# Kernel optimization log

Measured on AMD Instinct MI355X. Metric: run time of the kernel, lower is better.

The kernel has to match this reference:

```python
import jax, jax.numpy as jnp
import numpy as np

C = 256
RED = 2
C2 = C // RED


def setup_inputs() -> dict:
    key = jax.random.key(0)
    ks = jax.random.split(key, 6)
    B, H, W = 8, 64, 64
    x = jax.random.normal(ks[0], (B, C, H, W), dtype=jnp.float32)
    # 1x1 convs stored as [out_ch, in_ch] matrices
    W1 = jax.random.normal(ks[1], (C2, C), dtype=jnp.float32) * (1.0 / np.sqrt(C))
    b1 = jax.random.normal(ks[2], (C2,), dtype=jnp.float32) * 0.01
    W2 = jax.random.normal(ks[3], (C, C2), dtype=jnp.float32) * (1.0 / np.sqrt(C2))
    b2 = jax.random.normal(ks[4], (C,), dtype=jnp.float32) * 0.01
    # torch inits scale to zeros; use randn so the residual branch is active
    scale = jax.random.normal(ks[5], (1, C, 1, 1), dtype=jnp.float32)
    return {"x": x, "W1": W1, "b1": b1, "W2": W2, "b2": b2, "scale": scale}


def reference(x, W1, b1, W2, b2, scale):
    B, Cc, H, Wd = x.shape
    # conv1 (1x1): [B,C,H,W] -> [B,C2,H,W]
    y = jnp.einsum('bchw,oc->bohw', x, W1) + b1[None, :, None, None]
    # flatten spatial, move channels last: [B, N, C2]
    y = y.reshape(B, C2, H * Wd).transpose(0, 2, 1)
    # unscaled self-attention over N spatial positions
    att = jax.nn.softmax(jnp.einsum('bmc,bnc->bmn', y, y), axis=-1)  # [B,N,N]
    out = jnp.einsum('bmn,bnc->bmc', att, y)  # [B,N,C2]
    # faithful to torch: raw .view(B,-1,H,W) WITHOUT permuting back
    out = out.reshape(B, C2, H, Wd)
    # conv2 (1x1): [B,C2,H,W] -> [B,C,H,W]
    out = jnp.einsum('bchw,oc->bohw', out, W2) + b2[None, :, None, None]
    return out * scale + x
```

## Files before the change

### kernel.cpp

```cpp
#include <hip/hip_runtime.h>

#define B_  8
#define C_  256
#define C2_ 128
#define N_  4096
#define LOG2E 1.44269504088896f

typedef _Float16 f16;
typedef _Float16 f16x8 __attribute__((ext_vector_type(8)));
typedef float f32x4  __attribute__((ext_vector_type(4)));

__global__ __launch_bounds__(256)
void prep_kernel(const float* __restrict__ W1, const float* __restrict__ W2,
                 f16* __restrict__ w1h, f16* __restrict__ w2h)
{
  int i = blockIdx.x * 256 + threadIdx.x;
  w1h[i] = (f16)W1[i];
  w2h[i] = (f16)W2[i];
}

__global__ __launch_bounds__(256, 3)
void conv1_kernel(const float* __restrict__ x,
                  const f16* __restrict__ w1h,
                  const float* __restrict__ b1,
                  f16* __restrict__ Y, f16* __restrict__ Yt)
{
  __shared__ __align__(16) char smem[49152];
  float* Xr = (float*)smem;
  f16*   Ah = (f16*)(smem + 32768);
  f16*   T  = (f16*)smem;

  const int t = threadIdx.x;
  const int w = t >> 6, lane = t & 63, quad = lane >> 4, l16 = lane & 15;
  const int b = blockIdx.x, nt0 = blockIdx.y;

#pragma unroll
  for (int pass = 0; pass < 8; pass++) {
    int c  = (t >> 3) + pass * 32;
    int n4 = t & 7;
    float4 v = *(const float4*)(x + ((long)(b * C_ + c)) * N_ + nt0 * 32 + n4 * 4);
    *(float4*)(&Xr[c * 32 + (n4 ^ (c & 7)) * 4]) = v;
  }
  __syncthreads();
#pragma unroll
  for (int pass = 0; pass < 4; pass++) {
    int n  = t & 31;
    int kb = (t >> 5) + pass * 8;
    f16x8 vh;
#pragma unroll
    for (int jj = 0; jj < 8; jj++) {
      int cc = kb * 8 + jj;
      vh[jj] = (f16)Xr[cc * 32 + ((n >> 2) ^ (cc & 7)) * 4 + (n & 3)];
    }
    *(f16x8*)(&Ah[n * 256 + (kb ^ (n & 7)) * 8]) = vh;
  }
  __syncthreads();

  f16x8 bh[2][8];
#pragma unroll
  for (int nt = 0; nt < 2; nt++) {
    int c2 = w * 32 + nt * 16 + l16;
#pragma unroll
    for (int ks = 0; ks < 8; ks++)
      bh[nt][ks] = *(const f16x8*)(w1h + c2 * C_ + ks * 32 + quad * 8);
  }

  f32x4 acc[2][2];
#pragma unroll
  for (int i = 0; i < 2; i++)
#pragma unroll
    for (int j = 0; j < 2; j++) acc[i][j] = (f32x4){0.f, 0.f, 0.f, 0.f};

#pragma unroll
  for (int ks = 0; ks < 8; ks++)
#pragma unroll
    for (int mt = 0; mt < 2; mt++) {
      f16x8 ah = *(const f16x8*)(&Ah[(mt * 16 + l16) * 256 + (((ks * 4 + quad) ^ (l16 & 7))) * 8]);
#pragma unroll
      for (int nt = 0; nt < 2; nt++)
        acc[mt][nt] = __builtin_amdgcn_mfma_f32_16x16x32_f16(ah, bh[nt][ks], acc[mt][nt], 0, 0, 0);
    }
  __syncthreads();

#pragma unroll
  for (int nt = 0; nt < 2; nt++) {
    int c2 = w * 32 + nt * 16 + l16;
    float bv = b1[c2];
#pragma unroll
    for (int mt = 0; mt < 2; mt++)
#pragma unroll
      for (int rg = 0; rg < 4; rg++) {
        int n = mt * 16 + quad * 4 + rg;
        T[c2 * 40 + n] = (f16)(acc[mt][nt][rg] + bv);
      }
  }
  __syncthreads();
#pragma unroll
  for (int pass = 0; pass < 2; pass++) {
    int r  = (t >> 2) + pass * 64;
    int c8 = (t & 3) * 8;
    f16x8 v = *(const f16x8*)(&T[r * 40 + c8]);
    *(f16x8*)(Yt + ((long)(b * C2_ + r)) * N_ + nt0 * 32 + c8) = v;
  }
#pragma unroll
  for (int pass = 0; pass < 2; pass++) {
    int row = t & 31;
    int cg  = (t >> 5) + pass * 8;
    f16x8 v;
#pragma unroll
    for (int jj = 0; jj < 8; jj++) v[jj] = T[(cg * 8 + jj) * 40 + row];
    *(f16x8*)(Y + ((long)(b * N_ + nt0 * 32 + row)) * C2_ + cg * 8) = v;
  }
}

__global__ __launch_bounds__(256, 2)
void attn_kernel(const f16* __restrict__ Y, const f16* __restrict__ Yt,
                 f16* __restrict__ Op, float* __restrict__ ls)
{
  __shared__ f16 Ks[64 * 128];
  __shared__ f16 Vs[128 * 64];
  __shared__ f16 Ps[128 * 64];

  const int t = threadIdx.x;
  const int w = t >> 6, lane = t & 63, quad = lane >> 4, l16 = lane & 15;
  const int b = blockIdx.x, qt = blockIdx.y, s = blockIdx.z;
  const f16* Yb  = Y  + (long)b * N_ * C2_;
  const f16* Ytb = Yt + (long)b * C2_ * N_;
  const int kbase0 = s * 2048;

  f16x8 qf[2][4];
#pragma unroll
  for (int mt = 0; mt < 2; mt++)
#pragma unroll
    for (int ks = 0; ks < 4; ks++)
      qf[mt][ks] = *(const f16x8*)(Yb + (long)(qt * 128 + w * 32 + mt * 16 + l16) * C2_ + ks * 32 + quad * 8);

  {
    float* nsqf = (float*)Ps;
    int r = t >> 1, half = t & 1;
    float ss = 0.f;
#pragma unroll
    for (int j = 0; j < 8; j++) {
      f16x8 v = *(const f16x8*)(Yb + (long)(qt * 128 + r) * C2_ + half * 64 + j * 8);
#pragma unroll
      for (int e = 0; e < 8; e++) { float f = (float)v[e]; ss = fmaf(f, f, ss); }
    }
    ss += __shfl_xor(ss, 1);
    if (!(t & 1)) nsqf[r] = ss;
  }

#pragma unroll
  for (int pass = 0; pass < 4; pass++) {
    int r = (t >> 4) + pass * 16;
    f16x8 kv = *(const f16x8*)(Yb + (long)(kbase0 + r) * C2_ + (t & 15) * 8);
    *(f16x8*)(&Ks[r * 128 + (((t & 15)) ^ (r & 15)) * 8]) = kv;
  }
#pragma unroll
  for (int pass = 0; pass < 4; pass++) {
    int d = (t >> 3) + pass * 32;
    f16x8 vv = *(const f16x8*)(Ytb + (long)d * N_ + kbase0 + (t & 7) * 8);
    *(f16x8*)(&Vs[d * 64 + (((t & 7)) ^ (d & 7)) * 8]) = vv;
  }
  __syncthreads();

  float myns[2][4];
  {
    const float* nsqf = (const float*)Ps;
#pragma unroll
    for (int mt = 0; mt < 2; mt++)
#pragma unroll
      for (int rg = 0; rg < 4; rg++)
        myns[mt][rg] = nsqf[w * 32 + mt * 16 + quad * 4 + rg] * LOG2E;
  }
  __syncthreads();

  f16x8 ones;
#pragma unroll
  for (int j = 0; j < 8; j++) ones[j] = (f16)1.0f;

  f32x4 Oa[2][8];
#pragma unroll
  for (int i = 0; i < 2; i++)
#pragma unroll
    for (int j = 0; j < 8; j++) Oa[i][j] = (f32x4){0.f, 0.f, 0.f, 0.f};
  f32x4 lac[2] = {(f32x4){0.f,0.f,0.f,0.f}, (f32x4){0.f,0.f,0.f,0.f}};

#pragma unroll 1
  for (int kt = 0; kt < 32; kt++) {
    f16x8 stK[4], stV[4];
    if (kt + 1 < 32) {
      int nb = kbase0 + (kt + 1) * 64;
#pragma unroll
      for (int pass = 0; pass < 4; pass++)
        stK[pass] = *(const f16x8*)(Yb + (long)(nb + (t >> 4) + pass * 16) * C2_ + (t & 15) * 8);
#pragma unroll
      for (int pass = 0; pass < 4; pass++)
        stV[pass] = *(const f16x8*)(Ytb + (long)((t >> 3) + pass * 32) * N_ + nb + (t & 7) * 8);
    }

    f32x4 S[2][4];
#pragma unroll
    for (int i = 0; i < 2; i++)
#pragma unroll
      for (int j = 0; j < 4; j++) S[i][j] = (f32x4){0.f, 0.f, 0.f, 0.f};
#pragma unroll
    for (int ks = 0; ks < 4; ks++) {
      f16x8 bfr[4];
#pragma unroll
      for (int nt = 0; nt < 4; nt++)
        bfr[nt] = *(const f16x8*)(&Ks[(nt * 16 + l16) * 128 + (((ks * 4 + quad) ^ l16)) * 8]);
#pragma unroll
      for (int mt = 0; mt < 2; mt++)
#pragma unroll
        for (int nt = 0; nt < 4; nt++)
          S[mt][nt] = __builtin_amdgcn_mfma_f32_16x16x32_f16(qf[mt][ks], bfr[nt], S[mt][nt], 0, 0, 0);
    }

#pragma unroll
    for (int mt = 0; mt < 2; mt++)
#pragma unroll
      for (int rg = 0; rg < 4; rg++) {
        float nm = myns[mt][rg];
        int r = w * 32 + mt * 16 + quad * 4 + rg;
#pragma unroll
        for (int nt = 0; nt < 4; nt++) {
          float p = exp2f(fminf(fmaf(S[mt][nt][rg], LOG2E, -nm), 11.0f));
          int col = nt * 16 + l16;
          Ps[r * 64 + (((col >> 3) ^ (r & 7))) * 8 + (col & 7)] = (f16)p;
        }
      }

#pragma unroll
    for (int ks2 = 0; ks2 < 2; ks2++) {
      f16x8 vb[8];
#pragma unroll
      for (int dt = 0; dt < 8; dt++)
        vb[dt] = *(const f16x8*)(&Vs[(dt * 16 + l16) * 64 + (((ks2 * 4 + quad) ^ (l16 & 7))) * 8]);
      f16x8 pa[2];
#pragma unroll
      for (int mt = 0; mt < 2; mt++)
        pa[mt] = *(const f16x8*)(&Ps[(w * 32 + mt * 16 + l16) * 64 + (((ks2 * 4 + quad) ^ (l16 & 7))) * 8]);
#pragma unroll
      for (int mt = 0; mt < 2; mt++) {
#pragma unroll
        for (int dt = 0; dt < 8; dt++)
          Oa[mt][dt] = __builtin_amdgcn_mfma_f32_16x16x32_f16(pa[mt], vb[dt], Oa[mt][dt], 0, 0, 0);
        lac[mt] = __builtin_amdgcn_mfma_f32_16x16x32_f16(pa[mt], ones, lac[mt], 0, 0, 0);
      }
    }

    __syncthreads();
    if (kt + 1 < 32) {
#pragma unroll
      for (int pass = 0; pass < 4; pass++) {
        int r = (t >> 4) + pass * 16;
        *(f16x8*)(&Ks[r * 128 + (((t & 15)) ^ (r & 15)) * 8]) = stK[pass];
      }
#pragma unroll
      for (int pass = 0; pass < 4; pass++) {
        int d = (t >> 3) + pass * 32;
        *(f16x8*)(&Vs[d * 64 + (((t & 7)) ^ (d & 7)) * 8]) = stV[pass];
      }
    }
    __syncthreads();
  }

  const long rbase = ((long)s * B_ + b) * N_ + qt * 128;
#pragma unroll
  for (int mt = 0; mt < 2; mt++)
#pragma unroll
    for (int rg = 0; rg < 4; rg++) {
      int r = w * 32 + mt * 16 + quad * 4 + rg;
#pragma unroll
      for (int dt = 0; dt < 8; dt++)
        Op[(rbase + r) * C2_ + dt * 16 + l16] = (f16)Oa[mt][dt][rg];
      if (l16 == 0) ls[rbase + r] = lac[mt][rg];
    }
}

__global__ __launch_bounds__(256, 4)
void conv2_kernel(const f16* __restrict__ Op, const float* __restrict__ ls,
                  const f16* __restrict__ w2h,
                  const float* __restrict__ b2,
                  const float* __restrict__ scale,
                  const float* __restrict__ x,
                  float* __restrict__ out)
{
  __shared__ f16 Or[128 * 72];
  __shared__ f16 Bsw[64 * 128];
  __shared__ float invL[128];

  const int t = threadIdx.x;
  const int w = t >> 6, lane = t & 63, quad = lane >> 4, l16 = lane & 15;
  const int b = blockIdx.x, pt = blockIdx.y, oh = blockIdx.z;
  const long base0 = (long)b * 524288;
  const long base1 = 4194304 + base0;

  if (t < 128) {
    int q = t * 32 + (pt >> 1);
    float l = ls[(long)b * N_ + q] + ls[32768 + (long)b * N_ + q];
    invL[t] = 1.0f / fmaxf(l, 1e-20f);
  }
  __syncthreads();

#pragma unroll
  for (int pass = 0; pass < 4; pass++) {
    int j = (t >> 3) + pass * 32;
    int c8 = (t & 7) * 8;
    f16x8 a0 = *(const f16x8*)(Op + base0 + (long)j * N_ + pt * 64 + c8);
    f16x8 a1 = *(const f16x8*)(Op + base1 + (long)j * N_ + pt * 64 + c8);
    float iv = invL[j];
    f16x8 r;
#pragma unroll
    for (int jj = 0; jj < 8; jj++)
      r[jj] = (f16)(((float)a0[jj] + (float)a1[jj]) * iv);
    *(f16x8*)(&Or[j * 72 + c8]) = r;
  }
  __syncthreads();
#pragma unroll
  for (int pass = 0; pass < 4; pass++) {
    int p = t & 63;
    int q = (t >> 6) + pass * 4;
    f16x8 vv;
#pragma unroll
    for (int jj = 0; jj < 8; jj++) vv[jj] = Or[(q * 8 + jj) * 72 + p];
    *(f16x8*)(&Bsw[p * 128 + ((q ^ (p & 15))) * 8]) = vv;
  }
  __syncthreads();

  f32x4 acc[2][4];
#pragma unroll
  for (int i = 0; i < 2; i++)
#pragma unroll
    for (int j = 0; j < 4; j++) acc[i][j] = (f32x4){0.f, 0.f, 0.f, 0.f};

#pragma unroll
  for (int ks = 0; ks < 4; ks++) {
    f16x8 bfr[4];
#pragma unroll
    for (int nt = 0; nt < 4; nt++)
      bfr[nt] = *(const f16x8*)(&Bsw[(nt * 16 + l16) * 128 + (((ks * 4 + quad) ^ l16)) * 8]);
#pragma unroll
    for (int mt = 0; mt < 2; mt++) {
      int o = oh * 128 + w * 32 + mt * 16 + l16;
      f16x8 ah = *(const f16x8*)(w2h + o * C2_ + ks * 32 + quad * 8);
#pragma unroll
      for (int nt = 0; nt < 4; nt++)
        acc[mt][nt] = __builtin_amdgcn_mfma_f32_16x16x32_f16(ah, bfr[nt], acc[mt][nt], 0, 0, 0);
    }
  }
#pragma unroll
  for (int mt = 0; mt < 2; mt++)
#pragma unroll
    for (int rg = 0; rg < 4; rg++) {
      int o = oh * 128 + w * 32 + mt * 16 + quad * 4 + rg;
      float so = scale[o], bo = b2[o];
#pragma unroll
      for (int nt = 0; nt < 4; nt++) {
        int p = pt * 64 + nt * 16 + l16;
        long xo = ((long)b * C_ + o) * N_ + p;
        out[xo] = (acc[mt][nt][rg] + bo) * so + x[xo];
      }
    }
}

extern "C" void kernel_launch(void* const* d_in, const int* in_sizes, int n_in,
                              void* d_out, int out_size, void* d_ws, size_t ws_size,
                              hipStream_t stream) {
  const float* x     = (const float*)d_in[0];
  const float* W1    = (const float*)d_in[1];
  const float* b1    = (const float*)d_in[2];
  const float* W2    = (const float*)d_in[3];
  const float* b2    = (const float*)d_in[4];
  const float* scale = (const float*)d_in[5];
  float* outp = (float*)d_out;

  const size_t NE = (size_t)B_ * N_ * C2_;
  f16* Y   = (f16*)d_ws;
  f16* Yt  = Y + NE;
  f16* Op  = Yt + NE;
  float* ls = (float*)(Op + 2 * NE);
  f16* w1h = (f16*)(ls + 65536);
  f16* w2h = w1h + 32768;

  prep_kernel <<<dim3(128),      dim3(256), 0, stream>>>(W1, W2, w1h, w2h);
  conv1_kernel<<<dim3(8, 128),   dim3(256), 0, stream>>>(x, w1h, b1, Y, Yt);
  attn_kernel <<<dim3(8, 32, 2), dim3(256), 0, stream>>>(Y, Yt, Op, ls);
  conv2_kernel<<<dim3(8, 64, 2), dim3(256), 0, stream>>>(Op, ls, w2h, b2, scale, x, outp);
}
```

Baseline: 219.2 us.

## Keep softmax probabilities in registers by computing transposed scores for PV MFMA

The attention kernel now computes S^T (K as the A operand, Q as B) so each lane's accumulator layout matches the B-operand layout of a 16x16x16 MFMA. The exponentiated probabilities then feed the PV and row-sum MFMAs directly from registers, dropping the shared-memory P buffer, its stores and reloads, and one barrier. In exchange it issues twice as many smaller K=16 MFMAs for PV and reads V with narrower 4-element LDS loads. Output stores become vectorized f16x4.

```diff
diff --git a/kernel.cpp b/kernel.cpp
--- a/kernel.cpp
+++ b/kernel.cpp
@@ -7,6 +7,7 @@
 #define LOG2E 1.44269504088896f
 
 typedef _Float16 f16;
+typedef _Float16 f16x4 __attribute__((ext_vector_type(4)));
 typedef _Float16 f16x8 __attribute__((ext_vector_type(8)));
 typedef float f32x4  __attribute__((ext_vector_type(4)));
 
@@ -119,7 +120,7 @@
 {
   __shared__ f16 Ks[64 * 128];
   __shared__ f16 Vs[128 * 64];
-  __shared__ f16 Ps[128 * 64];
+  __shared__ float nsqf[128];
 
   const int t = threadIdx.x;
   const int w = t >> 6, lane = t & 63, quad = lane >> 4, l16 = lane & 15;
@@ -136,7 +137,6 @@
       qf[mt][ks] = *(const f16x8*)(Yb + (long)(qt * 128 + w * 32 + mt * 16 + l16) * C2_ + ks * 32 + quad * 8);
 
   {
-    float* nsqf = (float*)Ps;
     int r = t >> 1, half = t & 1;
     float ss = 0.f;
 #pragma unroll
@@ -146,7 +146,7 @@
       for (int e = 0; e < 8; e++) { float f = (float)v[e]; ss = fmaf(f, f, ss); }
     }
     ss += __shfl_xor(ss, 1);
-    if (!(t & 1)) nsqf[r] = ss;
+    if (!half) nsqf[r] = ss;
   }
 
 #pragma unroll
@@ -163,20 +163,11 @@
   }
   __syncthreads();
 
-  float myns[2][4];
-  {
-    const float* nsqf = (const float*)Ps;
-#pragma unroll
-    for (int mt = 0; mt < 2; mt++)
-#pragma unroll
-      for (int rg = 0; rg < 4; rg++)
-        myns[mt][rg] = nsqf[w * 32 + mt * 16 + quad * 4 + rg] * LOG2E;
-  }
-  __syncthreads();
-
-  f16x8 ones;
-#pragma unroll
-  for (int j = 0; j < 8; j++) ones[j] = (f16)1.0f;
+  float nm[2];
+  nm[0] = nsqf[w * 32 + l16] * LOG2E;
+  nm[1] = nsqf[w * 32 + 16 + l16] * LOG2E;
+
+  const f16x4 ones4 = {(f16)1.f, (f16)1.f, (f16)1.f, (f16)1.f};
 
   f32x4 Oa[2][8];
 #pragma unroll
@@ -198,11 +189,11 @@
         stV[pass] = *(const f16x8*)(Ytb + (long)((t >> 3) + pass * 32) * N_ + nb + (t & 7) * 8);
     }
 
-    f32x4 S[2][4];
-#pragma unroll
-    for (int i = 0; i < 2; i++)
-#pragma unroll
-      for (int j = 0; j < 4; j++) S[i][j] = (f32x4){0.f, 0.f, 0.f, 0.f};
+    f32x4 S[4][2];
+#pragma unroll
+    for (int i = 0; i < 4; i++)
+#pragma unroll
+      for (int j = 0; j < 2; j++) S[i][j] = (f32x4){0.f, 0.f, 0.f, 0.f};
 #pragma unroll
     for (int ks = 0; ks < 4; ks++) {
       f16x8 bfr[4];
@@ -210,42 +201,39 @@
       for (int nt = 0; nt < 4; nt++)
         bfr[nt] = *(const f16x8*)(&Ks[(nt * 16 + l16) * 128 + (((ks * 4 + quad) ^ l16)) * 8]);
 #pragma unroll
+      for (int nt = 0; nt < 4; nt++)
+#pragma unroll
+        for (int mt = 0; mt < 2; mt++)
+          S[nt][mt] = __builtin_amdgcn_mfma_f32_16x16x32_f16(bfr[nt], qf[mt][ks], S[nt][mt], 0, 0, 0);
+    }
+
+    f16x4 pb[4][2];
+#pragma unroll
+    for (int nt = 0; nt < 4; nt++)
+#pragma unroll
+      for (int mt = 0; mt < 2; mt++) {
+        f16x4 pv;
+#pragma unroll
+        for (int rg = 0; rg < 4; rg++)
+          pv[rg] = (f16)exp2f(fminf(fmaf(S[nt][mt][rg], LOG2E, -nm[mt]), 11.0f));
+        pb[nt][mt] = pv;
+      }
+
+#pragma unroll
+    for (int nt = 0; nt < 4; nt++)
+#pragma unroll
       for (int mt = 0; mt < 2; mt++)
-#pragma unroll
-        for (int nt = 0; nt < 4; nt++)
-          S[mt][nt] = __builtin_amdgcn_mfma_f32_16x16x32_f16(qf[mt][ks], bfr[nt], S[mt][nt], 0, 0, 0);
-    }
-
-#pragma unroll
-    for (int mt = 0; mt < 2; mt++)
-#pragma unroll
-      for (int rg = 0; rg < 4; rg++) {
-        float nm = myns[mt][rg];
-        int r = w * 32 + mt * 16 + quad * 4 + rg;
-#pragma unroll
-        for (int nt = 0; nt < 4; nt++) {
-          float p = exp2f(fminf(fmaf(S[mt][nt][rg], LOG2E, -nm), 11.0f));
-          int col = nt * 16 + l16;
-          Ps[r * 64 + (((col >> 3) ^ (r & 7))) * 8 + (col & 7)] = (f16)p;
-        }
-      }
-
-#pragma unroll
-    for (int ks2 = 0; ks2 < 2; ks2++) {
-      f16x8 vb[8];
-#pragma unroll
-      for (int dt = 0; dt < 8; dt++)
-        vb[dt] = *(const f16x8*)(&Vs[(dt * 16 + l16) * 64 + (((ks2 * 4 + quad) ^ (l16 & 7))) * 8]);
-      f16x8 pa[2];
-#pragma unroll
-      for (int mt = 0; mt < 2; mt++)
-        pa[mt] = *(const f16x8*)(&Ps[(w * 32 + mt * 16 + l16) * 64 + (((ks2 * 4 + quad) ^ (l16 & 7))) * 8]);
-#pragma unroll
-      for (int mt = 0; mt < 2; mt++) {
-#pragma unroll
-        for (int dt = 0; dt < 8; dt++)
-          Oa[mt][dt] = __builtin_amdgcn_mfma_f32_16x16x32_f16(pa[mt], vb[dt], Oa[mt][dt], 0, 0, 0);
-        lac[mt] = __builtin_amdgcn_mfma_f32_16x16x32_f16(pa[mt], ones, lac[mt], 0, 0, 0);
+        lac[mt] = __builtin_amdgcn_mfma_f32_16x16x16f16(ones4, pb[nt][mt], lac[mt], 0, 0, 0);
+
+#pragma unroll
+    for (int nt = 0; nt < 4; nt++) {
+#pragma unroll
+      for (int dt = 0; dt < 8; dt++) {
+        f16x4 va = *(const f16x4*)(&Vs[(dt * 16 + l16) * 64
+                      + (((nt * 2 + (quad >> 1)) ^ (l16 & 7))) * 8 + (quad & 1) * 4]);
+#pragma unroll
+        for (int mt = 0; mt < 2; mt++)
+          Oa[mt][dt] = __builtin_amdgcn_mfma_f32_16x16x16f16(va, pb[nt][mt], Oa[mt][dt], 0, 0, 0);
       }
     }
 
@@ -267,15 +255,16 @@
 
   const long rbase = ((long)s * B_ + b) * N_ + qt * 128;
 #pragma unroll
-  for (int mt = 0; mt < 2; mt++)
-#pragma unroll
-    for (int rg = 0; rg < 4; rg++) {
-      int r = w * 32 + mt * 16 + quad * 4 + rg;
-#pragma unroll
-      for (int dt = 0; dt < 8; dt++)
-        Op[(rbase + r) * C2_ + dt * 16 + l16] = (f16)Oa[mt][dt][rg];
-      if (l16 == 0) ls[rbase + r] = lac[mt][rg];
-    }
+  for (int mt = 0; mt < 2; mt++) {
+    int q = w * 32 + mt * 16 + l16;
+#pragma unroll
+    for (int dt = 0; dt < 8; dt++) {
+      f16x4 ov = {(f16)Oa[mt][dt][0], (f16)Oa[mt][dt][1],
+                  (f16)Oa[mt][dt][2], (f16)Oa[mt][dt][3]};
+      *(f16x4*)(Op + (rbase + q) * C2_ + dt * 16 + quad * 4) = ov;
+    }
+    if (quad == 0) ls[rbase + q] = lac[mt][0];
+  }
 }
 
 __global__ __launch_bounds__(256, 4)
```

New measurement: 225.5 us. +2.9%, slower.
